# Optimization experiments

Hardware: AMD Instinct MI355X
Metric: run time of the kernel (lower is better)

Reference implementation:

```python
import math
import jax, jax.numpy as jnp
import numpy as np

NUM_HEADS = 8
NUM_LANDMARKS = 64
MP_ITERS = 6


def moore_penrose_iter_pinv(x, iters=MP_ITERS):
    # x: [..., m, m]; iterative Newton-Schulz-style pseudo-inverse
    abs_x = jnp.abs(x)
    col = abs_x.sum(axis=-1)
    row = abs_x.sum(axis=-2)
    z = jnp.swapaxes(x, -1, -2) / (jnp.max(col) * jnp.max(row))
    I = jnp.eye(x.shape[-1], dtype=x.dtype)
    for _ in range(iters):
        xz = x @ z
        z = 0.25 * z @ (13.0 * I - xz @ (15.0 * I - xz @ (7.0 * I - xz)))
    return z


def setup_inputs() -> dict:
    key = jax.random.key(0)
    k_x, k_qkv, k_proj = jax.random.split(key, 3)
    B, T, E = 2, 2048, 512
    x = jax.random.normal(k_x, (B, T, E), dtype=jnp.float32)
    w_qkv = jax.random.normal(k_qkv, (E, 3 * E), dtype=jnp.float32) * 0.02
    b_qkv = jnp.zeros((3 * E,), dtype=jnp.float32)
    w_proj = jax.random.normal(k_proj, (E, E), dtype=jnp.float32) * 0.02
    b_proj = jnp.zeros((E,), dtype=jnp.float32)
    return {"x": x, "w_qkv": w_qkv, "b_qkv": b_qkv, "w_proj": w_proj, "b_proj": b_proj}


def reference(x, w_qkv, b_qkv, w_proj, b_proj):
    B, T, E = x.shape
    H = NUM_HEADS
    M = NUM_LANDMARKS
    hd = E // H
    # T chosen as a multiple of M so the original pad branch is a no-op
    qkv = x @ w_qkv + b_qkv  # [B,T,3E]
    q, k, v = jnp.split(qkv, 3, axis=-1)

    def to_heads(t):
        return t.reshape(B, T, H, hd).transpose(0, 2, 1, 3)  # [B,H,T,hd]

    q = to_heads(q) * (1.0 / math.sqrt(hd))
    k = to_heads(k)
    v = to_heads(v)

    l = T // M  # landmark group size
    q_landmarks = q.reshape(B, H, M, l, hd).mean(axis=3)  # [B,H,M,hd]
    k_landmarks = k.reshape(B, H, M, l, hd).mean(axis=3)  # [B,H,M,hd]

    q_kl = jnp.einsum('bhid,bhjd->bhij', q, k_landmarks)           # [B,H,T,M]
    ql_kl = jnp.einsum('bhid,bhjd->bhij', q_landmarks, k_landmarks)  # [B,H,M,M]
    ql_k = jnp.einsum('bhid,bhjd->bhij', q_landmarks, k)           # [B,H,M,T]

    neg_inf = float('-inf')
    mask_q_kl = jnp.tril(jnp.ones((T, M), dtype=bool))
    mask_ql_kl = jnp.tril(jnp.ones((M, M), dtype=bool))
    mask_ql_k = jnp.tril(jnp.ones((M, T), dtype=bool))

    F_t = jax.nn.softmax(jnp.where(mask_q_kl, q_kl, neg_inf), axis=-1)    # [B,H,T,M]
    A = jax.nn.softmax(jnp.where(mask_ql_kl, ql_kl, neg_inf), axis=-1)    # [B,H,M,M]
    B_t = jax.nn.softmax(jnp.where(mask_ql_k, ql_k, neg_inf), axis=-1)    # [B,H,M,T]

    A_t = moore_penrose_iter_pinv(A, iters=MP_ITERS)

    attn = (F_t @ A_t) @ B_t  # [B,H,T,T] (original materializes this for dropout)
    y = attn @ v              # [B,H,T,hd]
    y = y.transpose(0, 2, 1, 3).reshape(B, T, E)
    return y @ w_proj + b_proj
```

## Files before the change

### kernel.cpp

```cpp
#include <hip/hip_runtime.h>
#include <hip/hip_bf16.h>

#define TB 2048
#define EB 512

using short8 = __attribute__((ext_vector_type(8))) short;
using f32x4  = __attribute__((ext_vector_type(4))) float;

__global__ __launch_bounds__(256) void k_pool(const float* __restrict__ x,
                                              float* __restrict__ xp,
                                              unsigned int* __restrict__ scal_u) {
  if (blockIdx.x == 0 && threadIdx.x == 0) scal_u[0] = 0u;
  int idx = blockIdx.x * 256 + threadIdx.x;
  int b = idx >> 15;
  int rem = idx & 32767;
  int m = rem >> 9;
  int e = rem & 511;
  const float* src = x + (b * TB + m * 32) * EB + e;
  float s = 0.f;
#pragma unroll
  for (int i = 0; i < 32; ++i) s += src[i * EB];
  xp[idx] = s * (1.f / 32.f);
}

__device__ __forceinline__ int swz_idx(int row, int col) {
  return row * 64 + ((((col >> 3) ^ (row & 7)) << 3) | (col & 7));
}

__device__ __forceinline__ void split_bf(float v, ushort& h, ushort& l) {
  __hip_bfloat16 bh = __float2bfloat16(v);
  float fh = __bfloat162float(bh);
  __hip_bfloat16 bl = __float2bfloat16(v - fh);
  h = *(ushort*)&bh;
  l = *(ushort*)&bl;
}

__device__ __forceinline__ void mm_frags(const short8 ah[2], const short8 al[2],
                                         const ushort* bhp, const ushort* blp,
                                         int lane, f32x4 acc[4]) {
  const int g = lane >> 4, li = lane & 15;
#pragma unroll
  for (int nt = 0; nt < 4; ++nt) {
    f32x4 a = acc[nt];
#pragma unroll
    for (int kh = 0; kh < 2; ++kh) {
      int n = nt * 16 + li;
      int k0 = kh * 32 + 8 * g;
      int idx = n * 64 + ((((k0 >> 3) ^ (n & 7)) << 3));
      short8 bh = *(const short8*)&bhp[idx];
      short8 bl = *(const short8*)&blp[idx];
      a = __builtin_amdgcn_mfma_f32_16x16x32_bf16(al[kh], bh, a, 0, 0, 0);
      a = __builtin_amdgcn_mfma_f32_16x16x32_bf16(ah[kh], bl, a, 0, 0, 0);
      a = __builtin_amdgcn_mfma_f32_16x16x32_bf16(ah[kh], bh, a, 0, 0, 0);
    }
    acc[nt] = a;
  }
}

__device__ __forceinline__ void zero_acc(f32x4 acc[4]) {
#pragma unroll
  for (int nt = 0; nt < 4; ++nt) acc[nt] = (f32x4){0.f, 0.f, 0.f, 0.f};
}

__device__ __forceinline__ void softmax_rows(f32x4 s[4], int band, int g, int li,
                                             bool causal, int t0) {
#pragma unroll
  for (int r = 0; r < 4; ++r) {
    int trow = t0 + band + 4 * g + r;
    float m = -1e30f;
    float sv[4];
#pragma unroll
    for (int nt = 0; nt < 4; ++nt) {
      int col = nt * 16 + li;
      bool ok = !causal || (col <= trow);
      sv[nt] = ok ? s[nt][r] : -1e30f;
      m = fmaxf(m, sv[nt]);
    }
    m = fmaxf(m, __shfl_xor(m, 1));
    m = fmaxf(m, __shfl_xor(m, 2));
    m = fmaxf(m, __shfl_xor(m, 4));
    m = fmaxf(m, __shfl_xor(m, 8));
    float su = 0.f;
    float ee[4];
#pragma unroll
    for (int nt = 0; nt < 4; ++nt) {
      ee[nt] = (sv[nt] > -1e29f) ? __expf(sv[nt] - m) : 0.f;
      su += ee[nt];
    }
    su += __shfl_xor(su, 1);
    su += __shfl_xor(su, 2);
    su += __shfl_xor(su, 4);
    su += __shfl_xor(su, 8);
    float inv = 1.f / su;
#pragma unroll
    for (int nt = 0; nt < 4; ++nt) s[nt][r] = ee[nt] * inv;
  }
}

__device__ __forceinline__ void wrP(ushort* hp, ushort* lp, int lane,
                                    const f32x4 acc[4]) {
  const int g = lane >> 4, li = lane & 15;
#pragma unroll
  for (int nt = 0; nt < 4; ++nt) {
    int c = nt * 16 + li;
#pragma unroll
    for (int r = 0; r < 4; ++r) {
      int row = 4 * g + r;
      ushort h, l;
      split_bf(acc[nt][r], h, l);
      int idx = swz_idx(row, c);
      hp[idx] = h;
      lp[idx] = l;
    }
  }
}

__device__ __forceinline__ void ld_pfrags(const ushort* hp, const ushort* lp,
                                          int lane, short8 ah[2], short8 al[2]) {
  const int g = lane >> 4, li = lane & 15;
#pragma unroll
  for (int kh = 0; kh < 2; ++kh) {
    int k0 = kh * 32 + 8 * g;
    int idx = li * 64 + ((((k0 >> 3) ^ (li & 7)) << 3));
    ah[kh] = *(const short8*)&hp[idx];
    al[kh] = *(const short8*)&lp[idx];
  }
}

template <int MODE>
__global__ __launch_bounds__(256) void k_gemm_mfma(const float* __restrict__ A,
                                                   const float* __restrict__ A2,
                                                   const float* __restrict__ W,
                                                   const float* __restrict__ bias,
                                                   float* __restrict__ o0,
                                                   float* __restrict__ o1,
                                                   float* __restrict__ o2,
                                                   float* __restrict__ o3) {
  constexpr int LDW = (MODE == 1) ? 512 : 1536;
  __shared__ ushort Ah[4096], Al[4096], Bh[4096], Bl[4096];
  const int tid = threadIdx.x;
  const int lane = tid & 63, w = tid >> 6, band = w * 16;
  int bx, by;
  if constexpr (MODE == 0 || MODE == 1) {
    int bid = blockIdx.x;
    by = ((bid & 7) << 3) | (bid >> 6);
    bx = (bid >> 3) & 7;
  } else {
    bx = blockIdx.x;
    by = blockIdx.y;
  }
  const int variant = (MODE == 2) ? (by >> 1) : 0;
  const int m0 = (MODE == 2) ? ((by & 1) * 64) : by * 64;
  const int bcol0 = (MODE == 2) ? (variant == 0 ? 512 + bx * 64 : bx * 64)
                                : bx * 64;
  const int g = lane >> 4, li = lane & 15;

  const int arow = tid >> 2, akc = (tid & 3) * 16;
  const int bn = tid & 63, bkc = (tid >> 6) * 16;

  const float* asrc;
  {
    int gr = m0 + arow;
    if constexpr (MODE == 2) {
      asrc = (variant == 0) ? (A + ((gr >> 6) * TB + (gr & 63)) * EB)
                            : (A2 + gr * EB);
    } else {
      asrc = A + gr * EB;
    }
  }

  f32x4 acc[4];
  zero_acc(acc);

  float av[16], bv[16];
#pragma unroll
  for (int j = 0; j < 4; ++j)
    *(float4*)&av[j * 4] = *(const float4*)&asrc[akc + j * 4];
#pragma unroll
  for (int i = 0; i < 16; ++i) bv[i] = W[(bkc + i) * LDW + bcol0 + bn];

#pragma unroll
  for (int k0 = 0; k0 < 512; k0 += 64) {
    if (k0) __syncthreads();
#pragma unroll
    for (int c2 = 0; c2 < 2; ++c2) {
      short8 hv, lv;
#pragma unroll
      for (int i = 0; i < 8; ++i) {
        ushort h, l;
        split_bf(av[c2 * 8 + i], h, l);
        hv[i] = (short)h;
        lv[i] = (short)l;
      }
      int chunk = ((akc >> 3) + c2) ^ (arow & 7);
      int idx = arow * 64 + chunk * 8;
      *(short8*)&Ah[idx] = hv;
      *(short8*)&Al[idx] = lv;
    }
#pragma unroll
    for (int c2 = 0; c2 < 2; ++c2) {
      short8 hv, lv;
#pragma unroll
      for (int i = 0; i < 8; ++i) {
        ushort h, l;
        split_bf(bv[c2 * 8 + i], h, l);
        hv[i] = (short)h;
        lv[i] = (short)l;
      }
      int chunk = ((bkc >> 3) + c2) ^ (bn & 7);
      int idx = bn * 64 + chunk * 8;
      *(short8*)&Bh[idx] = hv;
      *(short8*)&Bl[idx] = lv;
    }
    __syncthreads();
    if (k0 + 64 < 512) {
#pragma unroll
      for (int j = 0; j < 4; ++j)
        *(float4*)&av[j * 4] = *(const float4*)&asrc[k0 + 64 + akc + j * 4];
#pragma unroll
      for (int i = 0; i < 16; ++i)
        bv[i] = W[(k0 + 64 + bkc + i) * LDW + bcol0 + bn];
    }
    short8 a_h[2], a_l[2];
    const int row = band + li;
#pragma unroll
    for (int kh = 0; kh < 2; ++kh) {
      int chunk = ((kh * 32 + 8 * g) >> 3) ^ (row & 7);
      int idx = row * 64 + chunk * 8;
      a_h[kh] = *(const short8*)&Ah[idx];
      a_l[kh] = *(const short8*)&Al[idx];
    }
    mm_frags(a_h, a_l, Bh, Bl, lane, acc);
  }
#pragma unroll
  for (int nt = 0; nt < 4; ++nt) {
#pragma unroll
    for (int r = 0; r < 4; ++r) {
      int trow = band + 4 * g + r;
      int gcol = bcol0 + nt * 16 + li;
      float v = acc[nt][r] + bias[gcol];
      if constexpr (MODE == 0) {
        int rg = m0 + trow;
        int b = rg >> 11, t = rg & 2047;
        int h = gcol >> 6, d = gcol & 63;
        o0[(((b << 3) | h) * 2048 + t) * 64 + d] = v * 0.125f;
      } else if constexpr (MODE == 1) {
        o0[(m0 + trow) * 512 + gcol] = v;
      } else {
        int gr = m0 + trow;
        int b = gr >> 6, t = gr & 63;
        int cloc = (variant == 0) ? (gcol - 512) : gcol;
        int which = cloc >> 9;
        int hd_ = cloc & 511;
        int h = hd_ >> 6, d = hd_ & 63;
        int dst = ((b * 8 + h) * 64 + t) * 64 + d;
        if (variant == 0) {
          if (which == 0) o0[dst] = v; else o1[dst] = v;
        } else {
          if (which == 0) o2[dst] = v * 0.125f; else o3[dst] = v;
        }
      }
    }
  }
}

__global__ __launch_bounds__(256) void k_a_bv_mfma(
    const float* __restrict__ qlg, const float* __restrict__ klg,
    const float* __restrict__ k64, const float* __restrict__ v64,
    float* __restrict__ A, float* __restrict__ BV,
    unsigned int* __restrict__ scal_u) {
  __shared__ ushort KLh[4096], KLl[4096], Kh[4096], Kl_[4096], VTh[4096], VTl[4096];
  __shared__ ushort Ph[4][1024], Pl[4][1024];
  __shared__ float red[4][64];
  const int bh = blockIdx.x, tid = threadIdx.x;
  const int lane = tid & 63, w = tid >> 6, band = w * 16;
  const int g = lane >> 4, li = lane & 15;
  const int base = bh * 4096;
  {
    int n = tid & 63, kc = (tid >> 6) * 16;
    float a[16], b[16], c[16];
#pragma unroll
    for (int i = 0; i < 16; ++i) {
      a[i] = klg[base + n * 64 + kc + i];
      b[i] = k64[base + n * 64 + kc + i];
      c[i] = v64[base + (kc + i) * 64 + n];
    }
#pragma unroll
    for (int c2 = 0; c2 < 2; ++c2) {
      int idx = n * 64 + ((((kc >> 3) + c2) ^ (n & 7)) << 3);
      short8 hv, lv;
#pragma unroll
      for (int i = 0; i < 8; ++i) { ushort h, l; split_bf(a[c2*8+i], h, l); hv[i]=(short)h; lv[i]=(short)l; }
      *(short8*)&KLh[idx] = hv; *(short8*)&KLl[idx] = lv;
#pragma unroll
      for (int i = 0; i < 8; ++i) { ushort h, l; split_bf(b[c2*8+i], h, l); hv[i]=(short)h; lv[i]=(short)l; }
      *(short8*)&Kh[idx] = hv; *(short8*)&Kl_[idx] = lv;
#pragma unroll
      for (int i = 0; i < 8; ++i) { ushort h, l; split_bf(c[c2*8+i], h, l); hv[i]=(short)h; lv[i]=(short)l; }
      *(short8*)&VTh[idx] = hv; *(short8*)&VTl[idx] = lv;
    }
  }
  short8 q_h[2], q_l[2];
  {
    int row = band + li;
#pragma unroll
    for (int kh = 0; kh < 2; ++kh) {
      int k0 = kh * 32 + 8 * g;
      float tmp[8];
      *(float4*)&tmp[0] = *(const float4*)&qlg[base + row * 64 + k0];
      *(float4*)&tmp[4] = *(const float4*)&qlg[base + row * 64 + k0 + 4];
      short8 hv, lv;
#pragma unroll
      for (int i = 0; i < 8; ++i) { ushort h, l; split_bf(tmp[i], h, l); hv[i]=(short)h; lv[i]=(short)l; }
      q_h[kh] = hv; q_l[kh] = lv;
    }
  }
  __syncthreads();
  f32x4 s1[4];
  zero_acc(s1);
  mm_frags(q_h, q_l, KLh, KLl, lane, s1);
  softmax_rows(s1, band, g, li, true, 0);
#pragma unroll
  for (int nt = 0; nt < 4; ++nt)
#pragma unroll
    for (int r = 0; r < 4; ++r)
      A[base + (band + 4 * g + r) * 64 + nt * 16 + li] = s1[nt][r];
  {
    float part[4];
#pragma unroll
    for (int nt = 0; nt < 4; ++nt) {
      part[nt] = s1[nt][0] + s1[nt][1] + s1[nt][2] + s1[nt][3];
      part[nt] += __shfl_xor(part[nt], 16);
      part[nt] += __shfl_xor(part[nt], 32);
    }
    if (g == 0) {
#pragma unroll
      for (int nt = 0; nt < 4; ++nt) red[w][nt * 16 + li] = part[nt];
    }
    __syncthreads();
    if (tid < 64) {
      float t = red[0][tid] + red[1][tid] + red[2][tid] + red[3][tid];
#pragma unroll
      for (int off = 32; off; off >>= 1) t = fmaxf(t, __shfl_xor(t, off));
      if (tid == 0) atomicMax(scal_u, __float_as_uint(t));
    }
  }
  f32x4 s2[4];
  zero_acc(s2);
  mm_frags(q_h, q_l, Kh, Kl_, lane, s2);
  softmax_rows(s2, band, g, li, true, 0);
  wrP(Ph[w], Pl[w], lane, s2);
  short8 p_h[2], p_l[2];
  ld_pfrags(Ph[w], Pl[w], lane, p_h, p_l);
  f32x4 y[4];
  zero_acc(y);
  mm_frags(p_h, p_l, VTh, VTl, lane, y);
#pragma unroll
  for (int nt = 0; nt < 4; ++nt)
#pragma unroll
    for (int r = 0; r < 4; ++r)
      BV[base + (band + 4 * g + r) * 64 + nt * 16 + li] = y[nt][r];
}

__device__ __forceinline__ void ld_afrags(const ushort* hp, const ushort* lp,
                                          int band, int lane,
                                          short8 ah[2], short8 al[2]) {
  const int g = lane >> 4, li = lane & 15;
  const int row = band + li;
#pragma unroll
  for (int kh = 0; kh < 2; ++kh) {
    int k0 = kh * 32 + 8 * g;
    int idx = row * 64 + ((((k0 >> 3) ^ (row & 7)) << 3));
    ah[kh] = *(const short8*)&hp[idx];
    al[kh] = *(const short8*)&lp[idx];
  }
}

__device__ __forceinline__ void mm_frags0(const short8 ah[2], const short8 al[2],
                                          const ushort* bhp, const ushort* blp,
                                          int lane, f32x4 acc[4]) {
  zero_acc(acc);
  mm_frags(ah, al, bhp, blp, lane, acc);
}

__device__ __forceinline__ void wrT(ushort* hp, ushort* lp, int band, int lane,
                                    const f32x4 acc[4], float cI, float mul) {
  const int g = lane >> 4, li = lane & 15;
  const int r0 = band + 4 * g;
#pragma unroll
  for (int nt = 0; nt < 4; ++nt) {
    int c = nt * 16 + li;
    ushort h[4], l[4];
#pragma unroll
    for (int r = 0; r < 4; ++r) {
      float v = mul * acc[nt][r] + ((r0 + r) == c ? cI : 0.f);
      split_bf(v, h[r], l[r]);
    }
    int idx = c * 64 + (((((r0) >> 3) ^ (c & 7)) << 3) | (r0 & 7));
    *(ushort4*)&hp[idx] = make_ushort4(h[0], h[1], h[2], h[3]);
    *(ushort4*)&lp[idx] = make_ushort4(l[0], l[1], l[2], l[3]);
  }
}

__device__ __forceinline__ void wrN(ushort* hp, ushort* lp, int band, int lane,
                                    const f32x4 acc[4], float mul) {
  const int g = lane >> 4, li = lane & 15;
#pragma unroll
  for (int nt = 0; nt < 4; ++nt) {
    int c = nt * 16 + li;
#pragma unroll
    for (int r = 0; r < 4; ++r) {
      int row = band + 4 * g + r;
      ushort h, l;
      split_bf(mul * acc[nt][r], h, l);
      int idx = swz_idx(row, c);
      hp[idx] = h;
      lp[idx] = l;
    }
  }
}

__global__ __launch_bounds__(256) void k_pinv(const float* __restrict__ A,
                                              const float* __restrict__ BVg,
                                              const unsigned int* __restrict__ scal_u,
                                              float* __restrict__ C) {
  __shared__ ushort ZT_h[4096], ZT_l[4096], ZA_h[4096], ZA_l[4096],
                    PA_h[4096], PA_l[4096], QA_h[4096], QA_l[4096],
                    QB_h[4096], QB_l[4096], BT_h[4096], BT_l[4096];
  const int bh = blockIdx.x, tid = threadIdx.x;
  const int lane = tid & 63, w = tid >> 6, band = w * 16;
  const int base = bh * 4096;
  const float sc = 1.f / __uint_as_float(scal_u[0]);
  const float* Ag = A + base;
  const float* Bg = BVg + base;

  {
    int prow = tid >> 2;
    int pc0 = (tid & 3) * 16;
#pragma unroll 4
    for (int j = 0; j < 16; ++j) {
      int col = pc0 + j;
      float av = Ag[prow * 64 + col] * sc;
      ushort h, l;
      split_bf(av, h, l);
      int i1 = swz_idx(prow, col);
      ZT_h[i1] = h; ZT_l[i1] = l;
      int i2 = swz_idx(col, prow);
      ZA_h[i2] = h; ZA_l[i2] = l;
      float bv = Bg[prow * 64 + col];
      split_bf(bv, h, l);
      BT_h[i2] = h; BT_l[i2] = l;
    }
  }
  short8 a_h[2], a_l[2];
  {
    const int g = lane >> 4, li = lane & 15;
    int row = band + li;
#pragma unroll
    for (int kh = 0; kh < 2; ++kh) {
      int k0 = kh * 32 + 8 * g;
      float tmp[8];
      *(float4*)&tmp[0] = *(const float4*)&Ag[row * 64 + k0];
      *(float4*)&tmp[4] = *(const float4*)&Ag[row * 64 + k0 + 4];
      short8 hv, lv;
#pragma unroll
      for (int i = 0; i < 8; ++i) {
        ushort h, l;
        split_bf(tmp[i], h, l);
        hv[i] = (short)h;
        lv[i] = (short)l;
      }
      a_h[kh] = hv;
      a_l[kh] = lv;
    }
  }
  __syncthreads();

  for (int it = 0; it < 6; ++it) {
    f32x4 acc[4];
    mm_frags0(a_h, a_l, ZT_h, ZT_l, lane, acc);
    wrN(PA_h, PA_l, band, lane, acc, 1.f);
    wrT(QA_h, QA_l, band, lane, acc, 7.f, -1.f);
    __syncthreads();
    short8 p_h[2], p_l[2];
    ld_afrags(PA_h, PA_l, band, lane, p_h, p_l);
    mm_frags0(p_h, p_l, QA_h, QA_l, lane, acc);
    wrT(QB_h, QB_l, band, lane, acc, 15.f, -1.f);
    __syncthreads();
    mm_frags0(p_h, p_l, QB_h, QB_l, lane, acc);
    wrT(QA_h, QA_l, band, lane, acc, 13.f, -1.f);
    __syncthreads();
    short8 z_h[2], z_l[2];
    ld_afrags(ZA_h, ZA_l, band, lane, z_h, z_l);
    mm_frags0(z_h, z_l, QA_h, QA_l, lane, acc);
    wrN(ZA_h, ZA_l, band, lane, acc, 0.25f);
    wrT(ZT_h, ZT_l, band, lane, acc, 0.f, 0.25f);
    __syncthreads();
  }
  {
    short8 z_h[2], z_l[2];
    ld_afrags(ZA_h, ZA_l, band, lane, z_h, z_l);
    f32x4 acc[4];
    mm_frags0(z_h, z_l, BT_h, BT_l, lane, acc);
    const int g = lane >> 4, li = lane & 15;
#pragma unroll
    for (int nt = 0; nt < 4; ++nt) {
#pragma unroll
      for (int r = 0; r < 4; ++r) {
        int row = band + 4 * g + r;
        int col = nt * 16 + li;
        C[base + row * 64 + col] = acc[nt][r];
      }
    }
  }
}

__global__ __launch_bounds__(256) void k_f_y_mfma(const float* __restrict__ q,
                                                  const float* __restrict__ klg,
                                                  const float* __restrict__ C,
                                                  float* __restrict__ yh) {
  __shared__ ushort KLh[4096], KLl[4096], CTh[4096], CTl[4096];
  __shared__ ushort Ph[4][1024], Pl[4][1024];
  const int bh = blockIdx.x;
  const int b = bh >> 3, h = bh & 7;
  const int t0 = blockIdx.y * 64;
  const int tid = threadIdx.x;
  const int lane = tid & 63, w = tid >> 6, band = w * 16;
  const int g = lane >> 4, li = lane & 15;
  const int base = bh * 4096;
  {
    int n = tid & 63, kc = (tid >> 6) * 16;
    float a[16], c[16];
#pragma unroll
    for (int i = 0; i < 16; ++i) {
      a[i] = klg[base + n * 64 + kc + i];
      c[i] = C[base + (kc + i) * 64 + n];
    }
#pragma unroll
    for (int c2 = 0; c2 < 2; ++c2) {
      int idx = n * 64 + ((((kc >> 3) + c2) ^ (n & 7)) << 3);
      short8 hv, lv;
#pragma unroll
      for (int i = 0; i < 8; ++i) { ushort hh, ll; split_bf(a[c2*8+i], hh, ll); hv[i]=(short)hh; lv[i]=(short)ll; }
      *(short8*)&KLh[idx] = hv; *(short8*)&KLl[idx] = lv;
#pragma unroll
      for (int i = 0; i < 8; ++i) { ushort hh, ll; split_bf(c[c2*8+i], hh, ll); hv[i]=(short)hh; lv[i]=(short)ll; }
      *(short8*)&CTh[idx] = hv; *(short8*)&CTl[idx] = lv;
    }
  }
  short8 q_h[2], q_l[2];
  {
    int t = t0 + band + li;
#pragma unroll
    for (int kh = 0; kh < 2; ++kh) {
      int k0 = kh * 32 + 8 * g;
      float tmp[8];
      *(float4*)&tmp[0] = *(const float4*)&q[(bh * 2048 + t) * 64 + k0];
      *(float4*)&tmp[4] = *(const float4*)&q[(bh * 2048 + t) * 64 + k0 + 4];
      short8 hv, lv;
#pragma unroll
      for (int i = 0; i < 8; ++i) { ushort hh, ll; split_bf(tmp[i], hh, ll); hv[i]=(short)hh; lv[i]=(short)ll; }
      q_h[kh] = hv; q_l[kh] = lv;
    }
  }
  __syncthreads();
  f32x4 s[4];
  zero_acc(s);
  mm_frags(q_h, q_l, KLh, KLl, lane, s);
  softmax_rows(s, band, g, li, blockIdx.y == 0, 0);
  wrP(Ph[w], Pl[w], lane, s);
  short8 p_h[2], p_l[2];
  ld_pfrags(Ph[w], Pl[w], lane, p_h, p_l);
  f32x4 y[4];
  zero_acc(y);
  mm_frags(p_h, p_l, CTh, CTl, lane, y);
#pragma unroll
  for (int nt = 0; nt < 4; ++nt)
#pragma unroll
    for (int r = 0; r < 4; ++r) {
      int t = t0 + band + 4 * g + r;
      int d = nt * 16 + li;
      yh[(b * 2048 + t) * 512 + h * 64 + d] = y[nt][r];
    }
}

extern "C" void kernel_launch(void* const* d_in, const int* in_sizes, int n_in,
                              void* d_out, int out_size, void* d_ws, size_t ws_size,
                              hipStream_t stream) {
  const float* x = (const float*)d_in[0];
  const float* w_qkv = (const float*)d_in[1];
  const float* b_qkv = (const float*)d_in[2];
  const float* w_proj = (const float*)d_in[3];
  const float* b_proj = (const float*)d_in[4];
  float* out = (float*)d_out;

  float* ws = (float*)d_ws;
  float* q = ws;
  float* k64 = q + 2097152;
  float* v64 = k64 + 65536;
  float* xp = v64 + 65536;
  float* ql = xp + 65536;
  float* kl = ql + 65536;
  float* Am = kl + 65536;
  float* BV = Am + 65536;
  float* Cm = BV + 65536;
  unsigned int* scal_u = (unsigned int*)(Cm + 65536);
  float* yh = (float*)(scal_u + 64);

  k_pool<<<dim3(256), dim3(256), 0, stream>>>(x, xp, scal_u);
  k_gemm_mfma<0><<<dim3(512), dim3(256), 0, stream>>>(x, nullptr, w_qkv, b_qkv,
                                                      q, nullptr, nullptr, nullptr);
  k_gemm_mfma<2><<<dim3(16, 4), dim3(256), 0, stream>>>(x, xp, w_qkv, b_qkv,
                                                        k64, v64, ql, kl);
  k_a_bv_mfma<<<dim3(16), dim3(256), 0, stream>>>(ql, kl, k64, v64, Am, BV, scal_u);
  k_pinv<<<dim3(16), dim3(256), 0, stream>>>(Am, BV, scal_u, Cm);
  k_f_y_mfma<<<dim3(16, 32), dim3(256), 0, stream>>>(q, kl, Cm, yh);
  k_gemm_mfma<1><<<dim3(512), dim3(256), 0, stream>>>(yh, nullptr, w_proj, b_proj,
                                                      out, nullptr, nullptr, nullptr);
}
```

Baseline: 143.8 us.

## Fold Q projection into landmark keys, compute scores directly from x

New measurement: 139.3 us. -3.1%, faster.

```diff
diff --git a/kernel.cpp b/kernel.cpp
--- a/kernel.cpp
+++ b/kernel.cpp
@@ -239,12 +239,7 @@
       int trow = band + 4 * g + r;
       int gcol = bcol0 + nt * 16 + li;
       float v = acc[nt][r] + bias[gcol];
-      if constexpr (MODE == 0) {
-        int rg = m0 + trow;
-        int b = rg >> 11, t = rg & 2047;
-        int h = gcol >> 6, d = gcol & 63;
-        o0[(((b << 3) | h) * 2048 + t) * 64 + d] = v * 0.125f;
-      } else if constexpr (MODE == 1) {
+      if constexpr (MODE == 1) {
         o0[(m0 + trow) * 512 + gcol] = v;
       } else {
         int gr = m0 + trow;
@@ -264,17 +259,86 @@
   }
 }
 
-__global__ __launch_bounds__(256) void k_a_bv_mfma(
+__global__ __launch_bounds__(256) void k_abv_w2(
     const float* __restrict__ qlg, const float* __restrict__ klg,
     const float* __restrict__ k64, const float* __restrict__ v64,
+    const float* __restrict__ w_qkv, const float* __restrict__ b_qkv,
     float* __restrict__ A, float* __restrict__ BV,
+    float* __restrict__ W2g, float* __restrict__ bcst,
     unsigned int* __restrict__ scal_u) {
   __shared__ ushort KLh[4096], KLl[4096], Kh[4096], Kl_[4096], VTh[4096], VTl[4096];
   __shared__ ushort Ph[4][1024], Pl[4][1024];
   __shared__ float red[4][64];
-  const int bh = blockIdx.x, tid = threadIdx.x;
+  const int tid = threadIdx.x;
   const int lane = tid & 63, w = tid >> 6, band = w * 16;
   const int g = lane >> 4, li = lane & 15;
+
+  if (blockIdx.x >= 16) {
+    const int bh = blockIdx.x - 16;
+    const int h = bh & 7;
+    const int base = bh * 4096;
+    {
+      int n = tid & 63, kc = (tid >> 6) * 16;
+      float a[16];
+#pragma unroll
+      for (int i = 0; i < 16; ++i) a[i] = klg[base + n * 64 + kc + i];
+#pragma unroll
+      for (int c2 = 0; c2 < 2; ++c2) {
+        int idx = n * 64 + ((((kc >> 3) + c2) ^ (n & 7)) << 3);
+        short8 hv, lv;
+#pragma unroll
+        for (int i = 0; i < 8; ++i) {
+          ushort hh, ll;
+          split_bf(a[c2 * 8 + i], hh, ll);
+          hv[i] = (short)hh;
+          lv[i] = (short)ll;
+        }
+        *(short8*)&KLh[idx] = hv;
+        *(short8*)&KLl[idx] = lv;
+      }
+    }
+    __syncthreads();
+    if (tid < 64) {
+      float bc = 0.f;
+      for (int d = 0; d < 64; ++d)
+        bc += b_qkv[h * 64 + d] * klg[base + tid * 64 + d];
+      bcst[bh * 64 + tid] = 0.125f * bc;
+    }
+#pragma unroll
+    for (int m0 = 0; m0 < 512; m0 += 64) {
+      short8 a_h[2], a_l[2];
+      int row = m0 + band + li;
+#pragma unroll
+      for (int kh = 0; kh < 2; ++kh) {
+        int d0 = kh * 32 + 8 * g;
+        float tmp[8];
+        *(float4*)&tmp[0] = *(const float4*)&w_qkv[row * 1536 + h * 64 + d0];
+        *(float4*)&tmp[4] = *(const float4*)&w_qkv[row * 1536 + h * 64 + d0 + 4];
+        short8 hv, lv;
+#pragma unroll
+        for (int i = 0; i < 8; ++i) {
+          ushort hh, ll;
+          split_bf(tmp[i], hh, ll);
+          hv[i] = (short)hh;
+          lv[i] = (short)ll;
+        }
+        a_h[kh] = hv;
+        a_l[kh] = lv;
+      }
+      f32x4 acc[4];
+      zero_acc(acc);
+      mm_frags(a_h, a_l, KLh, KLl, lane, acc);
+#pragma unroll
+      for (int nt = 0; nt < 4; ++nt)
+#pragma unroll
+        for (int r = 0; r < 4; ++r)
+          W2g[bh * 32768 + (m0 + band + 4 * g + r) * 64 + nt * 16 + li] =
+              0.125f * acc[nt][r];
+    }
+    return;
+  }
+
+  const int bh = blockIdx.x;
   const int base = bh * 4096;
   {
     int n = tid & 63, kc = (tid >> 6) * 16;
@@ -515,60 +579,119 @@
   }
 }
 
-__global__ __launch_bounds__(256) void k_f_y_mfma(const float* __restrict__ q,
-                                                  const float* __restrict__ klg,
-                                                  const float* __restrict__ C,
-                                                  float* __restrict__ yh) {
-  __shared__ ushort KLh[4096], KLl[4096], CTh[4096], CTl[4096];
+__global__ __launch_bounds__(256) void k_f_y2(const float* __restrict__ x,
+                                              const float* __restrict__ W2g,
+                                              const float* __restrict__ bcst,
+                                              const float* __restrict__ C,
+                                              float* __restrict__ yh) {
+  __shared__ ushort Ah[4096], Al[4096], Bh[4096], Bl[4096];
+  __shared__ ushort CTh[4096], CTl[4096];
   __shared__ ushort Ph[4][1024], Pl[4][1024];
-  const int bh = blockIdx.x;
-  const int b = bh >> 3, h = bh & 7;
-  const int t0 = blockIdx.y * 64;
   const int tid = threadIdx.x;
   const int lane = tid & 63, w = tid >> 6, band = w * 16;
-  const int g = lane >> 4, li = lane & 15;
+  const int bid = blockIdx.x;
+  const int by = ((bid & 7) << 3) | (bid >> 6);
+  const int bx = (bid >> 3) & 7;
+  const int b = by >> 5, t0 = (by & 31) * 64, h = bx;
+  const int bh = b * 8 + h;
+  const int g = lane >> 4, li = lane & 15;
+  const int arow = tid >> 2, akc = (tid & 3) * 16;
+  const int bn = tid & 63, bkc = (tid >> 6) * 16;
+  const float* asrc = x + (b * TB + t0 + arow) * EB;
+  const float* wsrc = W2g + bh * 32768;
   const int base = bh * 4096;
+
   {
     int n = tid & 63, kc = (tid >> 6) * 16;
-    float a[16], c[16];
-#pragma unroll
-    for (int i = 0; i < 16; ++i) {
-      a[i] = klg[base + n * 64 + kc + i];
-      c[i] = C[base + (kc + i) * 64 + n];
-    }
+    float c[16];
+#pragma unroll
+    for (int i = 0; i < 16; ++i) c[i] = C[base + (kc + i) * 64 + n];
 #pragma unroll
     for (int c2 = 0; c2 < 2; ++c2) {
       int idx = n * 64 + ((((kc >> 3) + c2) ^ (n & 7)) << 3);
       short8 hv, lv;
 #pragma unroll
-      for (int i = 0; i < 8; ++i) { ushort hh, ll; split_bf(a[c2*8+i], hh, ll); hv[i]=(short)hh; lv[i]=(short)ll; }
-      *(short8*)&KLh[idx] = hv; *(short8*)&KLl[idx] = lv;
-#pragma unroll
-      for (int i = 0; i < 8; ++i) { ushort hh, ll; split_bf(c[c2*8+i], hh, ll); hv[i]=(short)hh; lv[i]=(short)ll; }
-      *(short8*)&CTh[idx] = hv; *(short8*)&CTl[idx] = lv;
-    }
-  }
-  short8 q_h[2], q_l[2];
-  {
-    int t = t0 + band + li;
+      for (int i = 0; i < 8; ++i) {
+        ushort hh, ll;
+        split_bf(c[c2 * 8 + i], hh, ll);
+        hv[i] = (short)hh;
+        lv[i] = (short)ll;
+      }
+      *(short8*)&CTh[idx] = hv;
+      *(short8*)&CTl[idx] = lv;
+    }
+  }
+
+  f32x4 acc[4];
+  zero_acc(acc);
+  float av[16], bv[16];
+#pragma unroll
+  for (int j = 0; j < 4; ++j)
+    *(float4*)&av[j * 4] = *(const float4*)&asrc[akc + j * 4];
+#pragma unroll
+  for (int i = 0; i < 16; ++i) bv[i] = wsrc[(bkc + i) * 64 + bn];
+
+#pragma unroll
+  for (int k0 = 0; k0 < 512; k0 += 64) {
+    if (k0) __syncthreads();
+#pragma unroll
+    for (int c2 = 0; c2 < 2; ++c2) {
+      short8 hv, lv;
+#pragma unroll
+      for (int i = 0; i < 8; ++i) {
+        ushort hh, ll;
+        split_bf(av[c2 * 8 + i], hh, ll);
+        hv[i] = (short)hh;
+        lv[i] = (short)ll;
+      }
+      int chunk = ((akc >> 3) + c2) ^ (arow & 7);
+      int idx = arow * 64 + chunk * 8;
+      *(short8*)&Ah[idx] = hv;
+      *(short8*)&Al[idx] = lv;
+    }
+#pragma unroll
+    for (int c2 = 0; c2 < 2; ++c2) {
+      short8 hv, lv;
+#pragma unroll
+      for (int i = 0; i < 8; ++i) {
+        ushort hh, ll;
+        split_bf(bv[c2 * 8 + i], hh, ll);
+        hv[i] = (short)hh;
+        lv[i] = (short)ll;
+      }
+      int chunk = ((bkc >> 3) + c2) ^ (bn & 7);
+      int idx = bn * 64 + chunk * 8;
+      *(short8*)&Bh[idx] = hv;
+      *(short8*)&Bl[idx] = lv;
+    }
+    __syncthreads();
+    if (k0 + 64 < 512) {
+#pragma unroll
+      for (int j = 0; j < 4; ++j)
+        *(float4*)&av[j * 4] = *(const float4*)&asrc[k0 + 64 + akc + j * 4];
+#pragma unroll
+      for (int i = 0; i < 16; ++i)
+        bv[i] = wsrc[(k0 + 64 + bkc + i) * 64 + bn];
+    }
+    short8 a_h[2], a_l[2];
+    const int row = band + li;
 #pragma unroll
     for (int kh = 0; kh < 2; ++kh) {
-      int k0 = kh * 32 + 8 * g;
-      float tmp[8];
-      *(float4*)&tmp[0] = *(const float4*)&q[(bh * 2048 + t) * 64 + k0];
-      *(float4*)&tmp[4] = *(const float4*)&q[(bh * 2048 + t) * 64 + k0 + 4];
-      short8 hv, lv;
-#pragma unroll
-      for (int i = 0; i < 8; ++i) { ushort hh, ll; split_bf(tmp[i], hh, ll); hv[i]=(short)hh; lv[i]=(short)ll; }
-      q_h[kh] = hv; q_l[kh] = lv;
-    }
-  }
-  __syncthreads();
-  f32x4 s[4];
-  zero_acc(s);
-  mm_frags(q_h, q_l, KLh, KLl, lane, s);
-  softmax_rows(s, band, g, li, blockIdx.y == 0, 0);
-  wrP(Ph[w], Pl[w], lane, s);
+      int chunk = ((kh * 32 + 8 * g) >> 3) ^ (row & 7);
+      int idx = row * 64 + chunk * 8;
+      a_h[kh] = *(const short8*)&Ah[idx];
+      a_l[kh] = *(const short8*)&Al[idx];
+    }
+    mm_frags(a_h, a_l, Bh, Bl, lane, acc);
+  }
+#pragma unroll
+  for (int nt = 0; nt < 4; ++nt) {
+    float bc = bcst[bh * 64 + nt * 16 + li];
+#pragma unroll
+    for (int r = 0; r < 4; ++r) acc[nt][r] += bc;
+  }
+  softmax_rows(acc, band, g, li, t0 == 0, 0);
+  wrP(Ph[w], Pl[w], lane, acc);
   short8 p_h[2], p_l[2];
   ld_pfrags(Ph[w], Pl[w], lane, p_h, p_l);
   f32x4 y[4];
@@ -595,8 +718,9 @@
   float* out = (float*)d_out;
 
   float* ws = (float*)d_ws;
-  float* q = ws;
-  float* k64 = q + 2097152;
+  float* W2 = ws;
+  float* bcst = ws + 524288;
+  float* k64 = ws + 2097152;
   float* v64 = k64 + 65536;
   float* xp = v64 + 65536;
   float* ql = xp + 65536;
@@ -608,13 +732,12 @@
   float* yh = (float*)(scal_u + 64);
 
   k_pool<<<dim3(256), dim3(256), 0, stream>>>(x, xp, scal_u);
-  k_gemm_mfma<0><<<dim3(512), dim3(256), 0, stream>>>(x, nullptr, w_qkv, b_qkv,
-                                                      q, nullptr, nullptr, nullptr);
   k_gemm_mfma<2><<<dim3(16, 4), dim3(256), 0, stream>>>(x, xp, w_qkv, b_qkv,
                                                         k64, v64, ql, kl);
-  k_a_bv_mfma<<<dim3(16), dim3(256), 0, stream>>>(ql, kl, k64, v64, Am, BV, scal_u);
+  k_abv_w2<<<dim3(32), dim3(256), 0, stream>>>(ql, kl, k64, v64, w_qkv, b_qkv,
+                                               Am, BV, W2, bcst, scal_u);
   k_pinv<<<dim3(16), dim3(256), 0, stream>>>(Am, BV, scal_u, Cm);
-  k_f_y_mfma<<<dim3(16, 32), dim3(256), 0, stream>>>(q, kl, Cm, yh);
+  k_f_y2<<<dim3(512), dim3(256), 0, stream>>>(x, W2, bcst, Cm, yh);
   k_gemm_mfma<1><<<dim3(512), dim3(256), 0, stream>>>(yh, nullptr, w_proj, b_proj,
                                                       out, nullptr, nullptr, nullptr);
 }
```
